# Performance work log

Hardware: AMD Instinct MI355X
Metric: run time of the kernel (lower is better)

Reference implementation:

```python
import jax, jax.numpy as jnp
import numpy as np

B, S, E, H, T = 32, 512, 768, 128, 15  # H = hidden per direction (hidden_dim//2)


def setup_inputs() -> dict:
    key = jax.random.key(0)
    ks = jax.random.split(key, 16)
    sc = 1.0 / np.sqrt(H)
    inp = {
        "x": jax.random.normal(ks[0], (B, S, E), dtype=jnp.float32),
        "tags": jax.random.randint(ks[1], (B, S), 0, T),
        "mask": jnp.ones((B, S), dtype=jnp.int32),
        # forward-direction LSTM params (PyTorch gate order i,f,g,o)
        "Wih_f": jax.random.uniform(ks[2], (4 * H, E), minval=-sc, maxval=sc),
        "Whh_f": jax.random.uniform(ks[3], (4 * H, H), minval=-sc, maxval=sc),
        "bih_f": jax.random.uniform(ks[4], (4 * H,), minval=-sc, maxval=sc),
        "bhh_f": jax.random.uniform(ks[5], (4 * H,), minval=-sc, maxval=sc),
        # backward-direction LSTM params
        "Wih_b": jax.random.uniform(ks[6], (4 * H, E), minval=-sc, maxval=sc),
        "Whh_b": jax.random.uniform(ks[7], (4 * H, H), minval=-sc, maxval=sc),
        "bih_b": jax.random.uniform(ks[8], (4 * H,), minval=-sc, maxval=sc),
        "bhh_b": jax.random.uniform(ks[9], (4 * H,), minval=-sc, maxval=sc),
        # projection 2H -> T
        "Wp": jax.random.uniform(ks[10], (T, 2 * H), minval=-sc, maxval=sc),
        "bp": jax.random.uniform(ks[11], (T,), minval=-sc, maxval=sc),
        # CRF params (torchcrf: uniform(-0.1, 0.1))
        "trans": jax.random.uniform(ks[12], (T, T), minval=-0.1, maxval=0.1),
        "start_t": jax.random.uniform(ks[13], (T,), minval=-0.1, maxval=0.1),
        "end_t": jax.random.uniform(ks[14], (T,), minval=-0.1, maxval=0.1),
    }
    return inp


def _lstm_dir(xs, Wih, Whh, bih, bhh):
    """Single-direction LSTM over xs: (S, B, E) -> (S, B, H)."""
    h0 = jnp.zeros((xs.shape[1], Whh.shape[1]), xs.dtype)

    def step(carry, xt):
        h, c = carry
        z = xt @ Wih.T + h @ Whh.T + (bih + bhh)  # (B, 4H)
        i, f, g, o = jnp.split(z, 4, axis=-1)
        c = jax.nn.sigmoid(f) * c + jax.nn.sigmoid(i) * jnp.tanh(g)
        h = jax.nn.sigmoid(o) * jnp.tanh(c)
        return (h, c), h

    _, hs = jax.lax.scan(step, (h0, h0), xs)
    return hs


def _crf_nll(em, tg, mk, trans, start_t, end_t):
    """Negative log-likelihood, sum-reduced. em:(S,B,T) tg:(S,B) mk:(S,B) float."""
    b_idx = jnp.arange(em.shape[1])
    # --- numerator: score of the gold path ---
    em_tag = jnp.take_along_axis(em, tg[..., None], axis=2)[..., 0]  # (S, B)
    score = start_t[tg[0]] + em_tag[0]
    trans_sc = trans[tg[:-1], tg[1:]]  # (S-1, B)
    score = score + ((trans_sc + em_tag[1:]) * mk[1:]).sum(axis=0)
    seq_ends = mk.astype(jnp.int32).sum(axis=0) - 1  # (B,)
    last_tags = tg[seq_ends, b_idx]
    score = score + end_t[last_tags]
    # --- denominator: log partition via forward algorithm (scan) ---
    def fstep(alpha, inp):
        em_t, m_t = inp  # (B,T), (B,)
        nxt = jax.nn.logsumexp(alpha[:, :, None] + trans[None] + em_t[:, None, :], axis=1)
        alpha = jnp.where(m_t[:, None] > 0, nxt, alpha)
        return alpha, None

    alpha0 = start_t[None, :] + em[0]  # (B, T)
    alpha, _ = jax.lax.scan(fstep, alpha0, (em[1:], mk[1:]))
    logZ = jax.nn.logsumexp(alpha + end_t[None, :], axis=1)  # (B,)
    return -(score - logZ).sum()


def reference(x, tags, mask, Wih_f, Whh_f, bih_f, bhh_f, Wih_b, Whh_b, bih_b, bhh_b, Wp, bp, trans, start_t, end_t):
    xs = jnp.transpose(x, (1, 0, 2))  # (S, B, E)
    hf = _lstm_dir(xs, Wih_f, Whh_f, bih_f, bhh_f)
    hb = _lstm_dir(xs[::-1], Wih_b, Whh_b, bih_b, bhh_b)[::-1]
    h = jnp.concatenate([hf, hb], axis=-1)  # (S, B, 2H)
    em = h @ Wp.T + bp  # emissions (S, B, T)
    tg = tags.T  # (S, B)
    mk = mask.T.astype(em.dtype)
    return _crf_nll(em, tg, mk, trans, start_t, end_t)
```

## Files before the change

kernel.cpp:

```cpp
#include <hip/hip_runtime.h>
#include <hip/hip_bf16.h>
#include <cstdint>

typedef __attribute__((ext_vector_type(8))) short short8;
typedef __attribute__((ext_vector_type(4))) float f32x4;

#define NS 512
#define NB 32
#define NE 768
#define NH 128
#define NT 15
#define NM (NB*NS)

#define LOG2E  1.4426950408889634f
#define LOG2E2 2.8853900817779268f

__device__ __forceinline__ float bflo(unsigned int u){ return __builtin_bit_cast(float, u << 16); }
__device__ __forceinline__ float bfhi(unsigned int u){ return __builtin_bit_cast(float, u & 0xffff0000u); }
__device__ __forceinline__ float bfu(unsigned short u){ return __builtin_bit_cast(float, (unsigned)u << 16); }

__device__ __forceinline__ float rcpf_(float x){
#if __has_builtin(__builtin_amdgcn_rcpf)
  return __builtin_amdgcn_rcpf(x);
#else
  return __fdividef(1.f, x);
#endif
}
__device__ __forceinline__ float ex2_(float x){
#if __has_builtin(__builtin_amdgcn_exp2f)
  return __builtin_amdgcn_exp2f(x);
#else
  return exp2f(x);
#endif
}

__device__ __forceinline__ void lds_barrier() {
  asm volatile("s_waitcnt lgkmcnt(0)" ::: "memory");
  __builtin_amdgcn_s_barrier();
  asm volatile("" ::: "memory");
}

__device__ __forceinline__ void gload16(const void* g, void* l) {
#if __has_builtin(__builtin_amdgcn_global_load_lds)
  __builtin_amdgcn_global_load_lds((const __attribute__((address_space(1))) void*)g,
                                   (__attribute__((address_space(3))) void*)l, 16, 0, 0);
#else
  *(uint4*)l = *(const uint4*)g;
#endif
}

__device__ __forceinline__ float rdlane(float v, int i){
#if __has_builtin(__builtin_amdgcn_readlane)
  return __builtin_bit_cast(float, __builtin_amdgcn_readlane(__builtin_bit_cast(int, v), i));
#else
  return __shfl(v, i, 64);
#endif
}

__global__ void prep_all_kernel(
    const float* __restrict__ x,
    const float* __restrict__ wihf, const float* __restrict__ wihb,
    const float* __restrict__ whhf, const float* __restrict__ whhb,
    const float* __restrict__ bihf, const float* __restrict__ bhhf,
    const float* __restrict__ bihb, const float* __restrict__ bhhb,
    __hip_bfloat16* __restrict__ xbf,
    __hip_bfloat16* __restrict__ wihp,
    __hip_bfloat16* __restrict__ whhp,
    float* __restrict__ biasp)
{
  const int blk = blockIdx.x;
  if (blk < 2048) {
    const int n4 = NM*NE/4;
    int i = blk*256 + threadIdx.x;
    int stride = 2048*256;
    for (int j = i; j < n4; j += stride) {
      float4 v = ((const float4*)x)[j];
      ushort4 o;
      o.x = __builtin_bit_cast(unsigned short, __float2bfloat16(v.x));
      o.y = __builtin_bit_cast(unsigned short, __float2bfloat16(v.y));
      o.z = __builtin_bit_cast(unsigned short, __float2bfloat16(v.z));
      o.w = __builtin_bit_cast(unsigned short, __float2bfloat16(v.w));
      ((ushort4*)xbf)[j] = o;
    }
  } else {
    const int n = blk - 2048;
    const int dir = n >> 9, cc = n & 511, j = cc >> 2, g = cc & 3;
    const float fac = (g == 2) ? LOG2E2 : LOG2E;
    const int srow = g*128 + j;
    const float* si = (dir ? wihb : wihf) + (size_t)srow*768;
    __hip_bfloat16* di = wihp + (size_t)n*768;
    for (int e = threadIdx.x; e < 768; e += 256) di[e] = __float2bfloat16(si[e]*fac);
    const float* sh = (dir ? whhb : whhf) + (size_t)srow*128;
    __hip_bfloat16* dh = whhp + (size_t)n*128;
    if (threadIdx.x < 128) dh[threadIdx.x] = __float2bfloat16(sh[threadIdx.x]*fac);
    if (threadIdx.x == 0)
      biasp[n] = fac * (dir ? (bihb[srow] + bhhb[srow]) : (bihf[srow] + bhhf[srow]));
  }
}

__global__ __launch_bounds__(256, 4) void gemm_xproj(
    const __hip_bfloat16* __restrict__ A,
    const __hip_bfloat16* __restrict__ Bw,
    const float* __restrict__ biasp,
    __hip_bfloat16* __restrict__ xqd)
{
  __shared__ __align__(16) __hip_bfloat16 As[128*64];
  __shared__ __align__(16) __hip_bfloat16 Bs[128*64];
  const int id  = blockIdx.x;
  const int swzb = (id & 7)*128 + (id >> 3);
  const int bm = (swzb >> 3) * 128;
  const int bn = (swzb & 7) * 128;
  const int tid = threadIdx.x;
  const int lane = tid & 63;
  const int wv = tid >> 6;
  const int wr = wv >> 1, wc = wv & 1;
  char* AsB = (char*)As;
  char* BsB = (char*)Bs;
  const char* Ab = (const char*)A;
  const char* Bb = (const char*)Bw;
  f32x4 acc[4][4] = {};

  for (int kt = 0; kt < 12; ++kt) {
    const int k0 = kt * 64;
    __syncthreads();
    #pragma unroll
    for (int i = 0; i < 4; ++i) {
      int fb = i*4096 + tid*16;
      int r  = fb >> 7;
      int cb = fb & 127;
      int cbs = cb ^ ((r & 7) << 4);
      gload16(Ab + ((size_t)(bm + r)*768 + k0)*2 + cbs, AsB + fb);
      gload16(Bb + ((size_t)(bn + r)*768 + k0)*2 + cbs, BsB + fb);
    }
    __syncthreads();
    const int sw = ((lane & 7) << 4);
    #pragma unroll
    for (int ks = 0; ks < 2; ++ks) {
      const int krowb = ks*64 + ((lane >> 4) << 4);
      const int krows = krowb ^ sw;
      short8 af[4], bfr[4];
      #pragma unroll
      for (int m = 0; m < 4; ++m) {
        int row = wr*64 + m*16 + (lane & 15);
        af[m] = *(const short8*)(AsB + row*128 + krows);
      }
      #pragma unroll
      for (int n = 0; n < 4; ++n) {
        int row = wc*64 + n*16 + (lane & 15);
        bfr[n] = *(const short8*)(BsB + row*128 + krows);
      }
      #pragma unroll
      for (int m = 0; m < 4; ++m)
        #pragma unroll
        for (int n = 0; n < 4; ++n)
          acc[m][n] = __builtin_amdgcn_mfma_f32_16x16x32_bf16(af[m], bfr[n], acc[m][n], 0, 0, 0);
    }
  }
  #pragma unroll
  for (int m = 0; m < 4; ++m) {
    #pragma unroll
    for (int n = 0; n < 4; ++n) {
      const int col = bn + wc*64 + n*16 + (lane & 15);
      const float bv = biasp[col];
      const int dir = col >> 9;
      const int cc  = col & 511;
      #pragma unroll
      for (int jj = 0; jj < 4; ++jj) {
        const int row = bm + wr*64 + m*16 + ((lane >> 4)*4 + jj);
        xqd[((size_t)dir*NM + row)*512 + cc] = __float2bfloat16(acc[m][n][jj] + bv);
      }
    }
  }
}

__global__ __launch_bounds__(512) __attribute__((amdgpu_waves_per_eu(1, 2)))
void lstm_mfma(
    const __hip_bfloat16* __restrict__ xqd,
    const __hip_bfloat16* __restrict__ whhp,
    unsigned short* __restrict__ hf,
    unsigned short* __restrict__ hb)
{
  __shared__ __align__(16) char hfrag[2*4224];
  __shared__ __align__(16) float z_lds[4*520];

  const int bid = blockIdx.x;
  const int dir = bid >> 3, bg = bid & 7;
  const int t = threadIdx.x;
  const int w = t >> 6, l = t & 63;
  const int ln = l & 15, lp = l >> 4;

  uint4 afu[4][4];
  {
    const char* wbase = (const char*)(whhp + (size_t)dir*512*128);
    #pragma unroll
    for (int r = 0; r < 4; ++r) {
      const int row = (w*4 + r)*16 + ln;
      #pragma unroll
      for (int kc = 0; kc < 4; ++kc)
        afu[r][kc] = *(const uint4*)(wbase + ((size_t)row*128 + lp*8 + kc*32)*2);
    }
  }

  for (int i = t; i < 2*4224/4; i += 512) ((int*)hfrag)[i] = 0;

  const int b4 = t & 3, j = t >> 2;
  const int bsafe = bg*4 + b4;
  const int jsw = j ^ ((j >> 3) & 7);
  const int woff = (j >> 5)*1056 + ((j >> 3) & 3)*256 + b4*16 + (j & 7)*2;
  const int sdir = dir ? -1 : 1;
  const int s0 = dir ? 511 : 0;
  const ptrdiff_t xstep = (ptrdiff_t)sdir*512;
  const ptrdiff_t hstep = (ptrdiff_t)sdir*128;
  const __hip_bfloat16* xbase = xqd + ((size_t)dir*NM + (size_t)bsafe*512)*512
                                + (ptrdiff_t)s0*512 + j*4;
  unsigned short* hout = (dir ? hb : hf) + (size_t)bsafe*512*128 + (ptrdiff_t)s0*128 + j;

  float c = 0.f;

  uint2 x0 = *(const uint2*)(xbase);
  uint2 x1 = *(const uint2*)(xbase + xstep);
  uint2 x2 = *(const uint2*)(xbase + 2*xstep);
  uint2 x3 = *(const uint2*)(xbase + 3*xstep);
  const __hip_bfloat16* xpre = xbase + 4*xstep;
  __syncthreads();

  int buf = 0;

  auto STEP = [&](uint2& xc, bool pf) {
    short8 bfv[4];
    #pragma unroll
    for (int kc = 0; kc < 4; ++kc)
      bfv[kc] = *(const short8*)(hfrag + buf*4224 + kc*1056 + l*16);

    f32x4 acc[4];
    #pragma unroll
    for (int r = 0; r < 4; ++r) {
      acc[r] = f32x4{0.f, 0.f, 0.f, 0.f};
      #pragma unroll
      for (int kc = 0; kc < 4; ++kc)
        acc[r] = __builtin_amdgcn_mfma_f32_16x16x32_bf16(
                   __builtin_bit_cast(short8, afu[r][kc]), bfv[kc], acc[r], 0, 0, 0);
    }

    if (ln < 4) {
      #pragma unroll
      for (int r = 0; r < 4; ++r) {
        const int jw = (w*4 + r)*4 + lp;
        const int js = jw ^ ((jw >> 3) & 7);
        *(f32x4*)&z_lds[ln*520 + 4*js] = acc[r];
      }
    }
    lds_barrier();

    const f32x4 zv = *(const f32x4*)&z_lds[b4*520 + 4*jsw];
    const float zi = zv[0] + bflo(xc.x);
    const float zf = zv[1] + bfhi(xc.x);
    const float zg = zv[2] + bflo(xc.y);
    const float zo = zv[3] + bfhi(xc.y);
    const float I = rcpf_(1.f + ex2_(-zi));
    const float F = rcpf_(1.f + ex2_(-zf));
    const float G = 1.f - 2.f*rcpf_(ex2_(zg) + 1.f);
    const float O = rcpf_(1.f + ex2_(-zo));
    c = F*c + I*G;
    const float h = O*(1.f - 2.f*rcpf_(ex2_(c*LOG2E2) + 1.f));

    const unsigned short hbits =
        __builtin_bit_cast(unsigned short, __float2bfloat16(h));
    *(short*)(hfrag + (buf ^ 1)*4224 + woff) = (short)hbits;
    *hout = hbits;
    hout += hstep;

    if (pf) { xc = *(const uint2*)xpre; xpre += xstep; }
    lds_barrier();
    buf ^= 1;
  };

  for (int it = 0; it < 127; ++it) {
    #pragma unroll
    for (int r = 0; r < 4; ++r)
      #pragma unroll
      for (int kc = 0; kc < 4; ++kc)
        asm volatile("" : "+a"(afu[r][kc].x), "+a"(afu[r][kc].y),
                          "+a"(afu[r][kc].z), "+a"(afu[r][kc].w));
    STEP(x0, true);
    STEP(x1, true);
    STEP(x2, true);
    STEP(x3, true);
  }
  STEP(x0, false);
  STEP(x1, false);
  STEP(x2, false);
  STEP(x3, false);
}

__global__ __launch_bounds__(128) void em_kernel(
    const unsigned short* __restrict__ hf, const unsigned short* __restrict__ hb,
    const float* __restrict__ Wp, const float* __restrict__ bp,
    float* __restrict__ em)
{
  __shared__ float wps[15*256];
  __shared__ float bps[15];
  const int tid = threadIdx.x;
  for (int i = tid; i < 15*256; i += 128) wps[i] = Wp[i];
  if (tid < 15) bps[tid] = bp[tid];
  __syncthreads();
  const size_t m = (size_t)blockIdx.x*128 + tid;
  float acc[15];
  #pragma unroll
  for (int t2 = 0; t2 < 15; ++t2) acc[t2] = bps[t2];
  const ushort4* hf4 = (const ushort4*)(hf + m*128);
  const ushort4* hb4 = (const ushort4*)(hb + m*128);
  for (int kc = 0; kc < 32; ++kc) {
    const ushort4 hv = hf4[kc];
    const float h0 = bfu(hv.x), h1 = bfu(hv.y), h2 = bfu(hv.z), h3 = bfu(hv.w);
    #pragma unroll
    for (int t2 = 0; t2 < 15; ++t2)
      acc[t2] += h0*wps[t2*256 + kc*4+0] + h1*wps[t2*256 + kc*4+1]
               + h2*wps[t2*256 + kc*4+2] + h3*wps[t2*256 + kc*4+3];
  }
  for (int kc = 0; kc < 32; ++kc) {
    const ushort4 hv = hb4[kc];
    const float h0 = bfu(hv.x), h1 = bfu(hv.y), h2 = bfu(hv.z), h3 = bfu(hv.w);
    #pragma unroll
    for (int t2 = 0; t2 < 15; ++t2)
      acc[t2] += h0*wps[t2*256 + 128 + kc*4+0] + h1*wps[t2*256 + 128 + kc*4+1]
               + h2*wps[t2*256 + 128 + kc*4+2] + h3*wps[t2*256 + 128 + kc*4+3];
  }
  float* eo = em + m*15;
  #pragma unroll
  for (int t2 = 0; t2 < 15; ++t2) eo[t2] = acc[t2];
}

__global__ __launch_bounds__(64) void crf_chunks(
    const float* __restrict__ em,
    const int* __restrict__ mask,
    const float* __restrict__ trans,
    float* __restrict__ pmat)
{
  __shared__ float trs[240];
  __shared__ float cur[2][15][16];
  __shared__ float emc[16][16];
  __shared__ int mkc[16];
  const int b = blockIdx.x, cix = blockIdx.y;
  const int t = threadIdx.x;
  const int s0 = 1 + cix*16;
  const int ns = (512 - s0 < 16) ? (512 - s0) : 16;

  for (int e = t; e < 225; e += 64) trs[(e/15)*16 + (e%15)] = trans[e];
  for (int e = t; e < ns*15; e += 64) {
    const int k = e/15, j = e%15;
    emc[k][j] = em[((size_t)b*512 + s0 + k)*15 + j];
  }
  if (t < ns) mkc[t] = mask[b*512 + s0 + t];
  for (int e = t; e < 225; e += 64) {
    const int i = e/15, j = e%15;
    cur[0][i][j] = (i == j) ? 0.f : -1e30f;
  }
  __syncthreads();

  int cb = 0;
  for (int k = 0; k < ns; ++k) {
    if (mkc[k]) {
      for (int e = t; e < 225; e += 64) {
        const int i = e/15, j = e%15;
        float v[15];
        #pragma unroll
        for (int k2 = 0; k2 < 15; ++k2) v[k2] = cur[cb][i][k2] + trs[k2*16 + j];
        const float a01 = fmaxf(v[0], v[1]),  a23 = fmaxf(v[2], v[3]);
        const float a45 = fmaxf(v[4], v[5]),  a67 = fmaxf(v[6], v[7]);
        const float a89 = fmaxf(v[8], v[9]),  aab = fmaxf(v[10], v[11]);
        const float acd = fmaxf(v[12], v[13]);
        const float q0 = fmaxf(a01, a23), q1 = fmaxf(a45, a67);
        const float q2 = fmaxf(a89, aab), q3 = fmaxf(acd, v[14]);
        const float mx = fmaxf(fmaxf(q0, q1), fmaxf(q2, q3));
        float sum = 0.f;
        #pragma unroll
        for (int k2 = 0; k2 < 15; ++k2) sum += __expf(v[k2] - mx);
        cur[cb ^ 1][i][j] = emc[k][j] + mx + __logf(sum);
      }
      __syncthreads();
      cb ^= 1;
    }
  }
  float* P = pmat + ((size_t)b*32 + cix)*240;
  for (int e = t; e < 225; e += 64) {
    const int i = e/15, j = e%15;
    P[i*16 + j] = cur[cb][i][j];
  }
}

__global__ __launch_bounds__(64) void crf_final(
    const float* __restrict__ em,
    const float* __restrict__ pmat,
    const int* __restrict__ tags, const int* __restrict__ mask,
    const float* __restrict__ trans, const float* __restrict__ start_t,
    const float* __restrict__ end_t, float* __restrict__ nllb)
{
  __shared__ __align__(16) float ems[512*15];
  __shared__ float trs[225];
  __shared__ float Pl[240];
  __shared__ int tgs[512];
  __shared__ int mks[512];
  const int b = blockIdx.x, j = threadIdx.x;
  const float* emb = em + (size_t)b*512*15;
  {
    const float4* s4 = (const float4*)emb;
    float4* d4 = (float4*)ems;
    for (int i = j; i < 512*15/4; i += 64) d4[i] = s4[i];
    for (int i = j; i < 512; i += 64) { tgs[i] = tags[b*512+i]; mks[i] = mask[b*512+i]; }
    for (int i = j; i < 225; i += 64) trs[i] = trans[i];
  }
  __syncthreads();

  const int jc = (j < 15) ? j : 0;
  float alpha = (j < 15) ? (start_t[j] + ems[j]) : -1e30f;
  for (int cix = 0; cix < 32; ++cix) {
    const float* P = pmat + ((size_t)b*32 + cix)*240;
    __syncthreads();
    for (int e = j; e < 240; e += 64) Pl[e] = P[e];
    __syncthreads();
    float v[15];
    #pragma unroll
    for (int i = 0; i < 15; ++i) {
      const float ai = rdlane(alpha, i);
      v[i] = ai + Pl[i*16 + jc];
    }
    const float a01 = fmaxf(v[0], v[1]),  a23 = fmaxf(v[2], v[3]);
    const float a45 = fmaxf(v[4], v[5]),  a67 = fmaxf(v[6], v[7]);
    const float a89 = fmaxf(v[8], v[9]),  aab = fmaxf(v[10], v[11]);
    const float acd = fmaxf(v[12], v[13]);
    const float q0 = fmaxf(a01, a23), q1 = fmaxf(a45, a67);
    const float q2 = fmaxf(a89, aab), q3 = fmaxf(acd, v[14]);
    const float mx = fmaxf(fmaxf(q0, q1), fmaxf(q2, q3));
    float sum = 0.f;
    #pragma unroll
    for (int i = 0; i < 15; ++i) sum += __expf(v[i] - mx);
    const float nxt = mx + __logf(sum);
    if (j < 15) alpha = nxt;
  }

  float vz = (j < 15) ? (alpha + end_t[j]) : -1e30f;
  float mz = vz;
  #pragma unroll
  for (int off = 32; off > 0; off >>= 1) mz = fmaxf(mz, __shfl_xor(mz, off, 64));
  float se = (j < 15) ? __expf(vz - mz) : 0.f;
  #pragma unroll
  for (int off = 32; off > 0; off >>= 1) se += __shfl_xor(se, off, 64);
  const float logZ = mz + __logf(se);

  float sc = 0.f; int cnt = 0;
  for (int s = j; s < 512; s += 64) cnt += (mks[s] ? 1 : 0);
  for (int s = 1 + j; s < 512; s += 64) {
    if (mks[s]) {
      const int tp = tgs[s-1], tc = tgs[s];
      sc += trs[tp*15 + tc] + ems[s*15 + tc];
    }
  }
  #pragma unroll
  for (int off = 32; off > 0; off >>= 1) {
    sc  += __shfl_xor(sc, off, 64);
    cnt += __shfl_xor(cnt, off, 64);
  }
  if (j == 0) {
    const int t0 = tgs[0];
    sc += start_t[t0] + ems[t0];
    int last = cnt - 1; if (last < 0) last = 0;
    sc += end_t[tgs[last]];
    nllb[b] = logZ - sc;
  }
}

__global__ __launch_bounds__(64) void nll_reduce_kernel(const float* __restrict__ nllb,
                                                        float* __restrict__ out) {
  const int j = threadIdx.x;
  float v = (j < 32) ? nllb[j] : 0.f;
  #pragma unroll
  for (int off = 32; off > 0; off >>= 1) v += __shfl_xor(v, off, 64);
  if (j == 0) out[0] = v;
}

extern "C" void kernel_launch(void* const* d_in, const int* in_sizes, int n_in,
                              void* d_out, int out_size, void* d_ws, size_t ws_size,
                              hipStream_t stream) {
  const float* x      = (const float*)d_in[0];
  const int*   tags   = (const int*)d_in[1];
  const int*   mask   = (const int*)d_in[2];
  const float* Wih_f  = (const float*)d_in[3];
  const float* Whh_f  = (const float*)d_in[4];
  const float* bih_f  = (const float*)d_in[5];
  const float* bhh_f  = (const float*)d_in[6];
  const float* Wih_b  = (const float*)d_in[7];
  const float* Whh_b  = (const float*)d_in[8];
  const float* bih_b  = (const float*)d_in[9];
  const float* bhh_b  = (const float*)d_in[10];
  const float* Wp     = (const float*)d_in[11];
  const float* bp     = (const float*)d_in[12];
  const float* trans  = (const float*)d_in[13];
  const float* start_t= (const float*)d_in[14];
  const float* end_t  = (const float*)d_in[15];
  float* out = (float*)d_out;

  char* ws = (char*)d_ws;
  size_t off = 0;
  auto alloc = [&](size_t bytes) { char* p = ws + off; off += (bytes + 255) & ~(size_t)255; return p; };
  __hip_bfloat16* xbf   = (__hip_bfloat16*)alloc((size_t)NM*NE*2);
  __hip_bfloat16* Wihbf = (__hip_bfloat16*)alloc((size_t)1024*NE*2);
  __hip_bfloat16* whhp  = (__hip_bfloat16*)alloc((size_t)2*512*128*2);
  float*          biasp = (float*)alloc(1024*4);
  __hip_bfloat16* xqd   = (__hip_bfloat16*)alloc((size_t)2*NM*512*2);
  unsigned short* hf    = (unsigned short*)alloc((size_t)NM*128*2);
  unsigned short* hb    = (unsigned short*)alloc((size_t)NM*128*2);
  float*          em    = (float*)alloc((size_t)NM*15*4);
  float*          pmat  = (float*)alloc((size_t)32*32*240*4);
  float*          nllb  = (float*)alloc(32*4);
  (void)ws_size; (void)in_sizes; (void)n_in; (void)out_size;

  prep_all_kernel<<<3072, 256, 0, stream>>>(x, Wih_f, Wih_b, Whh_f, Whh_b,
                                            bih_f, bhh_f, bih_b, bhh_b,
                                            xbf, Wihbf, whhp, biasp);
  gemm_xproj<<<1024, 256, 0, stream>>>(xbf, Wihbf, biasp, xqd);
  lstm_mfma<<<16, 512, 0, stream>>>(xqd, whhp, hf, hb);
  em_kernel<<<128, 128, 0, stream>>>(hf, hb, Wp, bp, em);
  crf_chunks<<<dim3(32, 32), 64, 0, stream>>>(em, mask, trans, pmat);
  crf_final<<<32, 64, 0, stream>>>(em, pmat, tags, mask, trans, start_t, end_t, nllb);
  nll_reduce_kernel<<<1, 64, 0, stream>>>(nllb, out);
}
```

Measured before the change: 495.3 us.

## Replace MFMA LSTM recurrence with per-sequence fdot2 blocks in fp16

The recurrent LSTM kernel now gives each block a single batch sequence instead of four, launching 64 blocks where there were 16. The hidden-to-hidden matvec uses packed fp16 dot2 instructions, with each group of four lanes reducing through shuffles, in place of MFMA tiles that staged results through LDS. The intent is to spread the serial recurrence over more CUs and shorten the per-step critical path by dropping one LDS round trip and barrier. In exchange, recurrent weights are stored as fp16 rather than bf16, which changes rounding, and each thread now holds 64 weight registers.

```diff
diff --git a/kernel.cpp b/kernel.cpp
--- a/kernel.cpp
+++ b/kernel.cpp
@@ -4,6 +4,7 @@
 
 typedef __attribute__((ext_vector_type(8))) short short8;
 typedef __attribute__((ext_vector_type(4))) float f32x4;
+typedef _Float16 f16x2 __attribute__((ext_vector_type(2)));
 
 #define NS 512
 #define NB 32
@@ -18,6 +19,17 @@
 __device__ __forceinline__ float bflo(unsigned int u){ return __builtin_bit_cast(float, u << 16); }
 __device__ __forceinline__ float bfhi(unsigned int u){ return __builtin_bit_cast(float, u & 0xffff0000u); }
 __device__ __forceinline__ float bfu(unsigned short u){ return __builtin_bit_cast(float, (unsigned)u << 16); }
+
+__device__ __forceinline__ float fd2(unsigned int wp, unsigned int hp, float acc) {
+#if __has_builtin(__builtin_amdgcn_fdot2)
+  return __builtin_amdgcn_fdot2(__builtin_bit_cast(f16x2, wp),
+                                __builtin_bit_cast(f16x2, hp), acc, false);
+#else
+  f16x2 a = __builtin_bit_cast(f16x2, wp);
+  f16x2 b = __builtin_bit_cast(f16x2, hp);
+  return acc + (float)a[0]*(float)b[0] + (float)a[1]*(float)b[1];
+#endif
+}
 
 __device__ __forceinline__ float rcpf_(float x){
 #if __has_builtin(__builtin_amdgcn_rcpf)
@@ -65,7 +77,7 @@
     const float* __restrict__ bihb, const float* __restrict__ bhhb,
     __hip_bfloat16* __restrict__ xbf,
     __hip_bfloat16* __restrict__ wihp,
-    __hip_bfloat16* __restrict__ whhp,
+    _Float16* __restrict__ whhp,
     float* __restrict__ biasp)
 {
   const int blk = blockIdx.x;
@@ -91,8 +103,8 @@
     __hip_bfloat16* di = wihp + (size_t)n*768;
     for (int e = threadIdx.x; e < 768; e += 256) di[e] = __float2bfloat16(si[e]*fac);
     const float* sh = (dir ? whhb : whhf) + (size_t)srow*128;
-    __hip_bfloat16* dh = whhp + (size_t)n*128;
-    if (threadIdx.x < 128) dh[threadIdx.x] = __float2bfloat16(sh[threadIdx.x]*fac);
+    _Float16* dh = whhp + (size_t)n*128;
+    if (threadIdx.x < 128) dh[threadIdx.x] = (_Float16)(sh[threadIdx.x]*fac);
     if (threadIdx.x == 0)
       biasp[n] = fac * (dir ? (bihb[srow] + bhhb[srow]) : (bihf[srow] + bhhf[srow]));
   }
@@ -174,46 +186,47 @@
 }
 
 __global__ __launch_bounds__(512) __attribute__((amdgpu_waves_per_eu(1, 2)))
-void lstm_mfma(
+void lstm_fdot(
     const __hip_bfloat16* __restrict__ xqd,
-    const __hip_bfloat16* __restrict__ whhp,
+    const _Float16* __restrict__ whhp,
     unsigned short* __restrict__ hf,
     unsigned short* __restrict__ hb)
 {
-  __shared__ __align__(16) char hfrag[2*4224];
-  __shared__ __align__(16) float z_lds[4*520];
+  __shared__ __align__(16) _Float16 h_lds[2][128];
 
   const int bid = blockIdx.x;
-  const int dir = bid >> 3, bg = bid & 7;
+  const int dir = bid >> 5, b = bid & 31;
   const int t = threadIdx.x;
-  const int w = t >> 6, l = t & 63;
-  const int ln = l & 15, lp = l >> 4;
-
-  uint4 afu[4][4];
+  const int j = t >> 2, q = t & 3;
+
+  unsigned int wq[4][16];
   {
-    const char* wbase = (const char*)(whhp + (size_t)dir*512*128);
-    #pragma unroll
-    for (int r = 0; r < 4; ++r) {
-      const int row = (w*4 + r)*16 + ln;
+    const _Float16* wrow = whhp + ((size_t)dir*512 + j*4)*128 + q*32;
+    #pragma unroll
+    for (int g = 0; g < 4; ++g) {
+      const uint4* wp = (const uint4*)(wrow + g*128);
       #pragma unroll
-      for (int kc = 0; kc < 4; ++kc)
-        afu[r][kc] = *(const uint4*)(wbase + ((size_t)row*128 + lp*8 + kc*32)*2);
-    }
-  }
-
-  for (int i = t; i < 2*4224/4; i += 512) ((int*)hfrag)[i] = 0;
-
-  const int b4 = t & 3, j = t >> 2;
-  const int bsafe = bg*4 + b4;
-  const int jsw = j ^ ((j >> 3) & 7);
-  const int woff = (j >> 5)*1056 + ((j >> 3) & 3)*256 + b4*16 + (j & 7)*2;
+      for (int i = 0; i < 4; ++i) {
+        uint4 v = wp[i];
+        wq[g][i*4+0] = v.x; wq[g][i*4+1] = v.y; wq[g][i*4+2] = v.z; wq[g][i*4+3] = v.w;
+      }
+    }
+  }
+  #pragma unroll
+  for (int g = 0; g < 4; ++g)
+    #pragma unroll
+    for (int p = 0; p < 16; ++p)
+      asm volatile("" : "+v"(wq[g][p]));
+
+  if (t < 128) h_lds[0][t] = (_Float16)0.f;
+
   const int sdir = dir ? -1 : 1;
   const int s0 = dir ? 511 : 0;
   const ptrdiff_t xstep = (ptrdiff_t)sdir*512;
   const ptrdiff_t hstep = (ptrdiff_t)sdir*128;
-  const __hip_bfloat16* xbase = xqd + ((size_t)dir*NM + (size_t)bsafe*512)*512
+  const __hip_bfloat16* xbase = xqd + ((size_t)dir*NM + (size_t)b*512)*512
                                 + (ptrdiff_t)s0*512 + j*4;
-  unsigned short* hout = (dir ? hb : hf) + (size_t)bsafe*512*128 + (ptrdiff_t)s0*128 + j;
+  unsigned short* hout = (dir ? hb : hf) + (size_t)b*512*128 + (ptrdiff_t)s0*128 + j;
 
   float c = 0.f;
 
@@ -224,39 +237,31 @@
   const __hip_bfloat16* xpre = xbase + 4*xstep;
   __syncthreads();
 
-  int buf = 0;
+  int rb = 0;
 
   auto STEP = [&](uint2& xc, bool pf) {
-    short8 bfv[4];
-    #pragma unroll
-    for (int kc = 0; kc < 4; ++kc)
-      bfv[kc] = *(const short8*)(hfrag + buf*4224 + kc*1056 + l*16);
-
-    f32x4 acc[4];
-    #pragma unroll
-    for (int r = 0; r < 4; ++r) {
-      acc[r] = f32x4{0.f, 0.f, 0.f, 0.f};
-      #pragma unroll
-      for (int kc = 0; kc < 4; ++kc)
-        acc[r] = __builtin_amdgcn_mfma_f32_16x16x32_bf16(
-                   __builtin_bit_cast(short8, afu[r][kc]), bfv[kc], acc[r], 0, 0, 0);
-    }
-
-    if (ln < 4) {
-      #pragma unroll
-      for (int r = 0; r < 4; ++r) {
-        const int jw = (w*4 + r)*4 + lp;
-        const int js = jw ^ ((jw >> 3) & 7);
-        *(f32x4*)&z_lds[ln*520 + 4*js] = acc[r];
-      }
-    }
-    lds_barrier();
-
-    const f32x4 zv = *(const f32x4*)&z_lds[b4*520 + 4*jsw];
-    const float zi = zv[0] + bflo(xc.x);
-    const float zf = zv[1] + bfhi(xc.x);
-    const float zg = zv[2] + bflo(xc.y);
-    const float zo = zv[3] + bfhi(xc.y);
+    const uint4* h4 = (const uint4*)(&h_lds[rb][q*32]);
+    const uint4 hA = h4[0], hB = h4[1], hC = h4[2], hD = h4[3];
+    const unsigned int hq[16] = {hA.x,hA.y,hA.z,hA.w, hB.x,hB.y,hB.z,hB.w,
+                                 hC.x,hC.y,hC.z,hC.w, hD.x,hD.y,hD.z,hD.w};
+    float a0 = 0.f, a1 = 0.f, a2 = 0.f, a3 = 0.f;
+    #pragma unroll
+    for (int p = 0; p < 16; ++p) {
+      const unsigned int hv = hq[p];
+      a0 = fd2(wq[0][p], hv, a0);
+      a1 = fd2(wq[1][p], hv, a1);
+      a2 = fd2(wq[2][p], hv, a2);
+      a3 = fd2(wq[3][p], hv, a3);
+    }
+    a0 += __shfl_xor(a0, 1, 64); a1 += __shfl_xor(a1, 1, 64);
+    a2 += __shfl_xor(a2, 1, 64); a3 += __shfl_xor(a3, 1, 64);
+    a0 += __shfl_xor(a0, 2, 64); a1 += __shfl_xor(a1, 2, 64);
+    a2 += __shfl_xor(a2, 2, 64); a3 += __shfl_xor(a3, 2, 64);
+
+    const float zi = a0 + bflo(xc.x);
+    const float zf = a1 + bfhi(xc.x);
+    const float zg = a2 + bflo(xc.y);
+    const float zo = a3 + bfhi(xc.y);
     const float I = rcpf_(1.f + ex2_(-zi));
     const float F = rcpf_(1.f + ex2_(-zf));
     const float G = 1.f - 2.f*rcpf_(ex2_(zg) + 1.f);
@@ -264,24 +269,16 @@
     c = F*c + I*G;
     const float h = O*(1.f - 2.f*rcpf_(ex2_(c*LOG2E2) + 1.f));
 
-    const unsigned short hbits =
-        __builtin_bit_cast(unsigned short, __float2bfloat16(h));
-    *(short*)(hfrag + (buf ^ 1)*4224 + woff) = (short)hbits;
-    *hout = hbits;
+    if (q == 0)      h_lds[rb ^ 1][j] = (_Float16)h;
+    else if (q == 1) *hout = __builtin_bit_cast(unsigned short, __float2bfloat16(h));
     hout += hstep;
 
     if (pf) { xc = *(const uint2*)xpre; xpre += xstep; }
     lds_barrier();
-    buf ^= 1;
+    rb ^= 1;
   };
 
   for (int it = 0; it < 127; ++it) {
-    #pragma unroll
-    for (int r = 0; r < 4; ++r)
-      #pragma unroll
-      for (int kc = 0; kc < 4; ++kc)
-        asm volatile("" : "+a"(afu[r][kc].x), "+a"(afu[r][kc].y),
-                          "+a"(afu[r][kc].z), "+a"(afu[r][kc].w));
     STEP(x0, true);
     STEP(x1, true);
     STEP(x2, true);
@@ -505,7 +502,7 @@
   auto alloc = [&](size_t bytes) { char* p = ws + off; off += (bytes + 255) & ~(size_t)255; return p; };
   __hip_bfloat16* xbf   = (__hip_bfloat16*)alloc((size_t)NM*NE*2);
   __hip_bfloat16* Wihbf = (__hip_bfloat16*)alloc((size_t)1024*NE*2);
-  __hip_bfloat16* whhp  = (__hip_bfloat16*)alloc((size_t)2*512*128*2);
+  _Float16*       whhp  = (_Float16*)alloc((size_t)2*512*128*2);
   float*          biasp = (float*)alloc(1024*4);
   __hip_bfloat16* xqd   = (__hip_bfloat16*)alloc((size_t)2*NM*512*2);
   unsigned short* hf    = (unsigned short*)alloc((size_t)NM*128*2);
@@ -519,7 +516,7 @@
                                             bih_f, bhh_f, bih_b, bhh_b,
                                             xbf, Wihbf, whhp, biasp);
   gemm_xproj<<<1024, 256, 0, stream>>>(xbf, Wihbf, biasp, xqd);
-  lstm_mfma<<<16, 512, 0, stream>>>(xqd, whhp, hf, hb);
+  lstm_fdot<<<64, 512, 0, stream>>>(xqd, whhp, hf, hb);
   em_kernel<<<128, 128, 0, stream>>>(hf, hb, Wp, bp, em);
   crf_chunks<<<dim3(32, 32), 64, 0, stream>>>(em, mask, trans, pmat);
   crf_final<<<32, 64, 0, stream>>>(em, pmat, tags, mask, trans, start_t, end_t, nllb);
```

New measurement: 478.7 us. 1.03x faster.
